# Kernel optimization log

Measured on AMD Instinct MI355X. Metric: run time of the kernel, lower is better.

The kernel has to match this reference:

```python
import jax, jax.numpy as jnp
import numpy as np

EMBED_DIM = 768
NUM_HEADS = 12
HEAD_DIM = EMBED_DIM // NUM_HEADS
KERNEL = 7


def _neighbor_index(size, kernel):
    # NATTEN border-clamped neighborhood: window start = clip(i - k//2, 0, size-k)
    start = np.clip(np.arange(size) - kernel // 2, 0, size - kernel)
    return jnp.asarray(start[:, None] + np.arange(kernel)[None, :])  # [size, kernel]


def setup_inputs() -> dict:
    key = jax.random.key(0)
    k1, k2, k3, k4, k5 = jax.random.split(key, 5)
    B, H, W, C = 8, 64, 64, EMBED_DIM
    x = jax.random.normal(k1, (B, H, W, C), dtype=jnp.float32)
    # torch.nn.Linear layout: weight [out, in]
    w_qkv = jax.random.normal(k2, (3 * C, C), dtype=jnp.float32) * (C ** -0.5)
    b_qkv = jax.random.normal(k3, (3 * C,), dtype=jnp.float32) * 0.02
    w_proj = jax.random.normal(k4, (C, C), dtype=jnp.float32) * (C ** -0.5)
    b_proj = jax.random.normal(k5, (C,), dtype=jnp.float32) * 0.02
    return {"x": x, "w_qkv": w_qkv, "b_qkv": b_qkv, "w_proj": w_proj, "b_proj": b_proj}


def reference(x, w_qkv, b_qkv, w_proj, b_proj):
    B, H, W, C = x.shape
    scale = HEAD_DIM ** -0.5
    qkv = (x @ w_qkv.T + b_qkv).reshape(B, H, W, 3, NUM_HEADS, HEAD_DIM)
    q = qkv[..., 0, :, :] * scale          # [B,H,W,nh,hd]
    k = qkv[..., 1, :, :]
    v = qkv[..., 2, :, :]

    idx_i = _neighbor_index(H, KERNEL)      # [H,K]
    idx_j = _neighbor_index(W, KERNEL)      # [W,K]

    # Logits over the K*K local neighborhood, one shifted gather per offset
    # (avoids materializing [B,H,W,K2,nh,hd]).
    logits = []
    for ki in range(KERNEL):
        k_row = jnp.take(k, idx_i[:, ki], axis=1)          # [B,H,W,nh,hd]
        for kj in range(KERNEL):
            k_nb = jnp.take(k_row, idx_j[:, kj], axis=2)   # [B,H,W,nh,hd]
            logits.append(jnp.einsum('bhwnd,bhwnd->bhwn', q, k_nb))
    logits = jnp.stack(logits, axis=-1)                     # [B,H,W,nh,K2]
    attn = jax.nn.softmax(logits, axis=-1)

    out = jnp.zeros((B, H, W, NUM_HEADS, HEAD_DIM), dtype=x.dtype)
    off = 0
    for ki in range(KERNEL):
        v_row = jnp.take(v, idx_i[:, ki], axis=1)
        for kj in range(KERNEL):
            v_nb = jnp.take(v_row, idx_j[:, kj], axis=2)
            out = out + attn[..., off][..., None] * v_nb
            off += 1

    out = out.reshape(B, H, W, C)
    return out @ w_proj.T + b_proj
```

## Files before the change

kernel.cpp:

```cpp
#include <hip/hip_runtime.h>
#include <cstddef>

#define EMBED   768
#define NHEADS  12
#define HDIM    64
#define KSZ     7
#define IMG_H   64
#define IMG_W   64
#define BATCH   8
#define NTOK    (BATCH*IMG_H*IMG_W)
#define QKV_N   (3*EMBED)

typedef __attribute__((ext_vector_type(8))) short  bf16x8;
typedef __attribute__((ext_vector_type(4))) float  f32x4;
typedef __attribute__((ext_vector_type(8))) unsigned short u16x8;
typedef __attribute__((ext_vector_type(4))) unsigned short u16x4;

__device__ __forceinline__ unsigned short f2bf(float f) {
    unsigned int u = __float_as_uint(f);
    u += 0x7FFFu + ((u >> 16) & 1u);
    return (unsigned short)(u >> 16);
}

__device__ __forceinline__ void gload_lds16(const void* g, void* l) {
    __builtin_amdgcn_global_load_lds(
        (const __attribute__((address_space(1))) unsigned int*)g,
        (__attribute__((address_space(3))) unsigned int*)l, 16, 0, 0);
}

__global__ __launch_bounds__(256)
void cvt_bf16_kernel(const float* __restrict__ in, unsigned short* __restrict__ out, int n4)
{
    int i = blockIdx.x * 256 + threadIdx.x;
    if (i < n4) {
        float4 f = *(const float4*)(in + (size_t)i * 4);
        u16x4 o;
        o[0] = f2bf(f.x); o[1] = f2bf(f.y); o[2] = f2bf(f.z); o[3] = f2bf(f.w);
        *(u16x4*)(out + (size_t)i * 4) = o;
    }
}

template<int BF16OUT>
__global__ __launch_bounds__(256)
void mfma_gemm(const unsigned short* __restrict__ A, const unsigned short* __restrict__ W,
               const float* __restrict__ bias, void* __restrict__ outp,
               int N, int K, int scaleN, float scale)
{
    __shared__ unsigned short As[128 * 32];
    __shared__ unsigned short Bs[128 * 32];
    const int t = threadIdx.x;
    const int l = t & 63, w = t >> 6;
    const int bm = blockIdx.x * 128, bn = blockIdx.y * 128;
    const int wr = (w >> 1) * 64, wc = (w & 1) * 64;

    f32x4 acc[4][4] = {};

    const int srow = t >> 2;
    const int scol = (t & 3) * 8;
    unsigned short* ldsA0 = As + w * 512;
    unsigned short* ldsA1 = As + 2048 + w * 512;
    unsigned short* ldsB0 = Bs + w * 512;
    unsigned short* ldsB1 = Bs + 2048 + w * 512;
    const unsigned short* gA0 = A + (size_t)(bm + srow) * K + scol;
    const unsigned short* gA1 = A + (size_t)(bm + 64 + srow) * K + scol;
    const unsigned short* gB0 = W + (size_t)(bn + srow) * K + scol;
    const unsigned short* gB1 = W + (size_t)(bn + 64 + srow) * K + scol;

    const unsigned short* ra = As + (size_t)(wr + (l & 15)) * 32 + (l >> 4) * 8;
    const unsigned short* rb = Bs + (size_t)(wc + (l & 15)) * 32 + (l >> 4) * 8;

    for (int k0 = 0; k0 < K; k0 += 32) {
        __syncthreads();
        gload_lds16(gA0 + k0, ldsA0);
        gload_lds16(gA1 + k0, ldsA1);
        gload_lds16(gB0 + k0, ldsB0);
        gload_lds16(gB1 + k0, ldsB1);
        __syncthreads();
        bf16x8 af[4], bfr[4];
        #pragma unroll
        for (int i = 0; i < 4; ++i) af[i]  = *(const bf16x8*)(ra + i * 16 * 32);
        #pragma unroll
        for (int j = 0; j < 4; ++j) bfr[j] = *(const bf16x8*)(rb + j * 16 * 32);
        #pragma unroll
        for (int i = 0; i < 4; ++i)
            #pragma unroll
            for (int j = 0; j < 4; ++j)
                acc[i][j] = __builtin_amdgcn_mfma_f32_16x16x32_bf16(af[i], bfr[j], acc[i][j], 0, 0, 0);
    }

    const int cr = (l >> 4) * 4;
    const int cc = l & 15;
    #pragma unroll
    for (int i = 0; i < 4; ++i) {
        #pragma unroll
        for (int j = 0; j < 4; ++j) {
            const int col = bn + wc + j * 16 + cc;
            const float bv = bias[col];
            const bool sc = col < scaleN;
            #pragma unroll
            for (int r = 0; r < 4; ++r) {
                const int row = bm + wr + i * 16 + cr + r;
                float v = acc[i][j][r] + bv;
                if (sc) v *= scale;
                if (BF16OUT) ((unsigned short*)outp)[(size_t)row * N + col] = f2bf(v);
                else         ((float*)outp)[(size_t)row * N + col] = v;
            }
        }
    }
}

__global__ __launch_bounds__(256)
void natten_kernel(const unsigned short* __restrict__ qkv, unsigned short* __restrict__ attn_bf)
{
    __shared__ unsigned short smem[4 * 5888];
    const int t = threadIdx.x;
    const int w = t >> 6, l = t & 63;
    const int c15 = l & 15, g = l >> 4;
    const int blk = blockIdx.x;
    const int tg = blk & 15;
    const int h = (blk >> 4) % NHEADS;
    const int b = blk / (16 * NHEADS);
    const int ti = (tg >> 2) * 16, tj = (tg & 3) * 16;
    const int pi0 = ti + w * 4;
    const int ws = min(max(pi0 - 3, 0), IMG_H - 10);
    const int cs = min(max(tj - 3, 0), IMG_W - 22);
    const int pixbase = b * 4096;

    unsigned short* Kl = smem + w * 5888;
    unsigned short* Vt = Kl + 2304;

    const int pj = tj + c15;
    const int sj = min(max(pj - 3, 0), IMG_W - KSZ);
    const unsigned int cm = 0x7Fu << (sj - cs);
    unsigned int rm[4];
    #pragma unroll
    for (int qt = 0; qt < 4; ++qt) {
        int si = min(max(pi0 + qt - 3, 0), IMG_H - KSZ);
        rm[qt] = 0x7Fu << (si - ws);
    }

    bf16x8 qf[4][2];
    #pragma unroll
    for (int qt = 0; qt < 4; ++qt)
        #pragma unroll
        for (int dh = 0; dh < 2; ++dh)
            qf[qt][dh] = *(const bf16x8*)(qkv +
                (size_t)(pixbase + (pi0 + qt) * 64 + tj + c15) * QKV_N + h * HDIM + dh * 32 + g * 8);

    const int sr = l & 31;
    const int h5 = l >> 5;
    const int sig = ((sr & 12) << 1) | ((sr & 16) >> 2) | (sr & 3);

    u16x8 kst[4], vst[4];

    {
        int ur = sr / 22, uc = sr - ur * 22;
        int prow = min(ws + ur, IMG_H - 1);
        const u16x8* gk = (const u16x8*)(qkv +
            (size_t)(pixbase + prow * 64 + cs + uc) * QKV_N + EMBED + h * HDIM + h5 * 32);
        #pragma unroll
        for (int i = 0; i < 4; ++i) { kst[i] = gk[i]; vst[i] = gk[i + 96]; }
    }
    #pragma unroll
    for (int i = 0; i < 4; ++i) *(u16x8*)(Kl + sr * 72 + h5 * 32 + i * 8) = kst[i];
    #pragma unroll
    for (int i = 0; i < 4; ++i)
        #pragma unroll
        for (int e = 0; e < 8; ++e)
            Vt[(h5 * 32 + i * 8 + e) * 56 + sig] = vst[i][e];

    f32x4 oacc[4][4] = {};
    float spart[4] = {0.f, 0.f, 0.f, 0.f};

    #pragma unroll 1
    for (int C = 0; C < 7; ++C) {
        if (C < 6) {
            int kk = (C + 1) * 32 + sr;
            int ur = kk / 22, uc = kk - ur * 22;
            int prow = min(ws + ur, IMG_H - 1);
            const u16x8* gk = (const u16x8*)(qkv +
                (size_t)(pixbase + prow * 64 + cs + uc) * QKV_N + EMBED + h * HDIM + h5 * 32);
            #pragma unroll
            for (int i = 0; i < 4; ++i) { kst[i] = gk[i]; vst[i] = gk[i + 96]; }
        }

        bf16x8 ka[2][2], vb[4];
        #pragma unroll
        for (int kt = 0; kt < 2; ++kt)
            #pragma unroll
            for (int dh = 0; dh < 2; ++dh)
                ka[kt][dh] = *(const bf16x8*)(Kl + (kt * 16 + c15) * 72 + dh * 32 + g * 8);
        #pragma unroll
        for (int dt = 0; dt < 4; ++dt)
            vb[dt] = *(const bf16x8*)(Vt + (dt * 16 + c15) * 56 + g * 8);

        int kk0 = C * 32 + 4 * g;
        int a22 = kk0 / 22;
        int uc0 = kk0 - a22 * 22;
        int urx[2][4]; unsigned int cb[2][4];
        #pragma unroll
        for (int kt = 0; kt < 2; ++kt)
            #pragma unroll
            for (int r = 0; r < 4; ++r) {
                int x = uc0 + kt * 16 + r;
                int wrp = x >= 22;
                int uc = x - (wrp ? 22 : 0);
                urx[kt][r] = a22 + wrp;
                cb[kt][r] = (cm >> uc) & 1u;
            }

        #pragma unroll
        for (int qt = 0; qt < 4; ++qt) {
            f32x4 s0 = {}, s1 = {};
            s0 = __builtin_amdgcn_mfma_f32_16x16x32_bf16(ka[0][0], qf[qt][0], s0, 0, 0, 0);
            s0 = __builtin_amdgcn_mfma_f32_16x16x32_bf16(ka[0][1], qf[qt][1], s0, 0, 0, 0);
            s1 = __builtin_amdgcn_mfma_f32_16x16x32_bf16(ka[1][0], qf[qt][0], s1, 0, 0, 0);
            s1 = __builtin_amdgcn_mfma_f32_16x16x32_bf16(ka[1][1], qf[qt][1], s1, 0, 0, 0);
            float p[2][4];
            #pragma unroll
            for (int r = 0; r < 4; ++r) {
                float e0 = exp2f(s0[r]);
                float e1 = exp2f(s1[r]);
                p[0][r] = ((rm[qt] >> urx[0][r]) & cb[0][r]) ? e0 : 0.f;
                p[1][r] = ((rm[qt] >> urx[1][r]) & cb[1][r]) ? e1 : 0.f;
                spart[qt] += p[0][r] + p[1][r];
            }
            unsigned int pk[4];
            asm("v_cvt_pk_bf16_f32 %0, %1, %2" : "=v"(pk[0]) : "v"(p[0][0]), "v"(p[0][1]));
            asm("v_cvt_pk_bf16_f32 %0, %1, %2" : "=v"(pk[1]) : "v"(p[0][2]), "v"(p[0][3]));
            asm("v_cvt_pk_bf16_f32 %0, %1, %2" : "=v"(pk[2]) : "v"(p[1][0]), "v"(p[1][1]));
            asm("v_cvt_pk_bf16_f32 %0, %1, %2" : "=v"(pk[3]) : "v"(p[1][2]), "v"(p[1][3]));
            bf16x8 pa = *(bf16x8*)pk;
            #pragma unroll
            for (int dt = 0; dt < 4; ++dt)
                oacc[qt][dt] = __builtin_amdgcn_mfma_f32_16x16x32_bf16(pa, vb[dt], oacc[qt][dt], 0, 0, 0);
        }

        if (C < 6) {
            #pragma unroll
            for (int i = 0; i < 4; ++i) *(u16x8*)(Kl + sr * 72 + h5 * 32 + i * 8) = kst[i];
            #pragma unroll
            for (int i = 0; i < 4; ++i)
                #pragma unroll
                for (int e = 0; e < 8; ++e)
                    Vt[(h5 * 32 + i * 8 + e) * 56 + sig] = vst[i][e];
        }
    }

    #pragma unroll
    for (int qt = 0; qt < 4; ++qt) {
        float s = spart[qt];
        s += __shfl_xor(s, 16);
        s += __shfl_xor(s, 32);
        #pragma unroll
        for (int r = 0; r < 4; ++r) {
            float sb = __shfl(s, 4 * g + r);
            float inv = __builtin_amdgcn_rcpf(sb);
            size_t obase = (size_t)(pixbase + (pi0 + qt) * 64 + tj + 4 * g + r) * EMBED
                         + h * HDIM + c15;
            #pragma unroll
            for (int dt = 0; dt < 4; ++dt)
                attn_bf[obase + dt * 16] = f2bf(oacc[qt][dt][r] * inv);
        }
    }
}

extern "C" void kernel_launch(void* const* d_in, const int* in_sizes, int n_in,
                              void* d_out, int out_size, void* d_ws, size_t ws_size,
                              hipStream_t stream)
{
    const float* x      = (const float*)d_in[0];
    const float* w_qkv  = (const float*)d_in[1];
    const float* b_qkv  = (const float*)d_in[2];
    const float* w_proj = (const float*)d_in[3];
    const float* b_proj = (const float*)d_in[4];
    float* out = (float*)d_out;

    char* p = (char*)d_ws;
    unsigned short* qkv = (unsigned short*)p;     p += (size_t)NTOK * QKV_N * 2;
    unsigned short* xbf = (unsigned short*)p;
    unsigned short* attn_bf = xbf;                p += (size_t)NTOK * EMBED * 2;
    unsigned short* wq_bf = (unsigned short*)p;   p += (size_t)QKV_N * EMBED * 2;
    unsigned short* wp_bf = (unsigned short*)p;

    const float scale = 0.125f * 1.44269504088896f;

    {
        int n4 = NTOK * EMBED / 4;
        cvt_bf16_kernel<<<(n4 + 255) / 256, 256, 0, stream>>>(x, xbf, n4);
        n4 = QKV_N * EMBED / 4;
        cvt_bf16_kernel<<<(n4 + 255) / 256, 256, 0, stream>>>(w_qkv, wq_bf, n4);
        n4 = EMBED * EMBED / 4;
        cvt_bf16_kernel<<<(n4 + 255) / 256, 256, 0, stream>>>(w_proj, wp_bf, n4);
    }

    {
        dim3 g1(NTOK / 128, QKV_N / 128);
        mfma_gemm<1><<<g1, 256, 0, stream>>>(xbf, wq_bf, b_qkv, qkv, QKV_N, EMBED, EMBED, scale);
    }

    natten_kernel<<<BATCH * NHEADS * 16, 256, 0, stream>>>(qkv, attn_bf);

    {
        dim3 g2(NTOK / 128, EMBED / 128);
        mfma_gemm<0><<<g2, 256, 0, stream>>>(attn_bf, wp_bf, b_proj, out, EMBED, EMBED, 0, 1.0f);
    }
}
```

Before: 359.1 us.

## Double-buffer GEMM LDS tiles and use lane-contiguous fragment layout

The MFMA GEMM now keeps two LDS buffers and prefetches the next K-slice through direct global-to-LDS loads while computing on the current one, so only one barrier per iteration is needed. The LDS layout also changes so that each 16-row fragment is stored lane-contiguously, letting each lane read its bf16x8 operand at l*8 and avoiding strided bank conflicts. In exchange, LDS use doubles, which may lower occupancy. Correctness depends on the async load into the other buffer being ordered against the trailing barrier.

```diff
diff --git a/kernel.cpp b/kernel.cpp
--- a/kernel.cpp
+++ b/kernel.cpp
@@ -46,46 +46,56 @@
                const float* __restrict__ bias, void* __restrict__ outp,
                int N, int K, int scaleN, float scale)
 {
-    __shared__ unsigned short As[128 * 32];
-    __shared__ unsigned short Bs[128 * 32];
+    __shared__ unsigned short As[2 * 4096];
+    __shared__ unsigned short Bs[2 * 4096];
     const int t = threadIdx.x;
     const int l = t & 63, w = t >> 6;
     const int bm = blockIdx.x * 128, bn = blockIdx.y * 128;
     const int wr = (w >> 1) * 64, wc = (w & 1) * 64;
 
+    const int r16 = l & 15, kg = l >> 4;
+    const unsigned short* gA0 = A + (size_t)(bm + w * 16 + r16) * K + kg * 8;
+    const unsigned short* gA1 = A + (size_t)(bm + (w + 4) * 16 + r16) * K + kg * 8;
+    const unsigned short* gB0 = W + (size_t)(bn + w * 16 + r16) * K + kg * 8;
+    const unsigned short* gB1 = W + (size_t)(bn + (w + 4) * 16 + r16) * K + kg * 8;
+    unsigned short* lA0 = As + w * 512;
+    unsigned short* lA1 = As + (w + 4) * 512;
+    unsigned short* lB0 = Bs + w * 512;
+    unsigned short* lB1 = Bs + (w + 4) * 512;
+
+    const unsigned short* ra = As + ((wr >> 4)) * 512 + l * 8;
+    const unsigned short* rb = Bs + ((wc >> 4)) * 512 + l * 8;
+
     f32x4 acc[4][4] = {};
-
-    const int srow = t >> 2;
-    const int scol = (t & 3) * 8;
-    unsigned short* ldsA0 = As + w * 512;
-    unsigned short* ldsA1 = As + 2048 + w * 512;
-    unsigned short* ldsB0 = Bs + w * 512;
-    unsigned short* ldsB1 = Bs + 2048 + w * 512;
-    const unsigned short* gA0 = A + (size_t)(bm + srow) * K + scol;
-    const unsigned short* gA1 = A + (size_t)(bm + 64 + srow) * K + scol;
-    const unsigned short* gB0 = W + (size_t)(bn + srow) * K + scol;
-    const unsigned short* gB1 = W + (size_t)(bn + 64 + srow) * K + scol;
-
-    const unsigned short* ra = As + (size_t)(wr + (l & 15)) * 32 + (l >> 4) * 8;
-    const unsigned short* rb = Bs + (size_t)(wc + (l & 15)) * 32 + (l >> 4) * 8;
-
-    for (int k0 = 0; k0 < K; k0 += 32) {
-        __syncthreads();
-        gload_lds16(gA0 + k0, ldsA0);
-        gload_lds16(gA1 + k0, ldsA1);
-        gload_lds16(gB0 + k0, ldsB0);
-        gload_lds16(gB1 + k0, ldsB1);
-        __syncthreads();
+    const int NT = K / 32;
+
+    gload_lds16(gA0, lA0);
+    gload_lds16(gA1, lA1);
+    gload_lds16(gB0, lB0);
+    gload_lds16(gB1, lB1);
+    __syncthreads();
+
+    for (int ts = 0; ts < NT; ++ts) {
+        const int cur = (ts & 1) * 4096;
+        if (ts + 1 < NT) {
+            const int nk = (ts + 1) * 32;
+            const int nb = ((ts + 1) & 1) * 4096;
+            gload_lds16(gA0 + nk, lA0 + nb);
+            gload_lds16(gA1 + nk, lA1 + nb);
+            gload_lds16(gB0 + nk, lB0 + nb);
+            gload_lds16(gB1 + nk, lB1 + nb);
+        }
         bf16x8 af[4], bfr[4];
         #pragma unroll
-        for (int i = 0; i < 4; ++i) af[i]  = *(const bf16x8*)(ra + i * 16 * 32);
-        #pragma unroll
-        for (int j = 0; j < 4; ++j) bfr[j] = *(const bf16x8*)(rb + j * 16 * 32);
+        for (int i = 0; i < 4; ++i) af[i]  = *(const bf16x8*)(ra + cur + i * 512);
+        #pragma unroll
+        for (int j = 0; j < 4; ++j) bfr[j] = *(const bf16x8*)(rb + cur + j * 512);
         #pragma unroll
         for (int i = 0; i < 4; ++i)
             #pragma unroll
             for (int j = 0; j < 4; ++j)
                 acc[i][j] = __builtin_amdgcn_mfma_f32_16x16x32_bf16(af[i], bfr[j], acc[i][j], 0, 0, 0);
+        __syncthreads();
     }
 
     const int cr = (l >> 4) * 4;
```

New measurement: 427.4 us. 1.19x slower.

## Replace GEMM with 256x256-tile triple-buffered pipelined MFMA kernel

Applied to the files above, without the earlier changes.

Replaces the 128x128 single-buffered GEMM with a 256x256 tile, 512-thread kernel. It uses a three-stage LDS ring with direct global-to-LDS prefetch two k-steps ahead, XOR swizzling against bank conflicts, split MFMA phases with s_setprio, and a swizzled block order for L2 locality. The aim is to hide global load latency behind MFMA work and raise arithmetic intensity for both projection GEMMs. In exchange it uses more registers and 96KB of LDS, and the synchronization relies on manual vmcnt waits.

```diff
diff --git a/kernel.cpp b/kernel.cpp
--- a/kernel.cpp
+++ b/kernel.cpp
@@ -41,66 +41,99 @@
 }
 
 template<int BF16OUT>
-__global__ __launch_bounds__(256)
-void mfma_gemm(const unsigned short* __restrict__ A, const unsigned short* __restrict__ W,
-               const float* __restrict__ bias, void* __restrict__ outp,
-               int N, int K, int scaleN, float scale)
+__global__ __launch_bounds__(512)
+void gemm256(const unsigned short* __restrict__ A, const unsigned short* __restrict__ W,
+             const float* __restrict__ bias, void* __restrict__ outp,
+             int M, int N, int K, int scaleN, float scale)
 {
-    __shared__ unsigned short As[128 * 32];
-    __shared__ unsigned short Bs[128 * 32];
-    const int t = threadIdx.x;
-    const int l = t & 63, w = t >> 6;
-    const int bm = blockIdx.x * 128, bn = blockIdx.y * 128;
-    const int wr = (w >> 1) * 64, wc = (w & 1) * 64;
-
-    f32x4 acc[4][4] = {};
-
-    const int srow = t >> 2;
-    const int scol = (t & 3) * 8;
-    unsigned short* ldsA0 = As + w * 512;
-    unsigned short* ldsA1 = As + 2048 + w * 512;
-    unsigned short* ldsB0 = Bs + w * 512;
-    unsigned short* ldsB1 = Bs + 2048 + w * 512;
-    const unsigned short* gA0 = A + (size_t)(bm + srow) * K + scol;
-    const unsigned short* gA1 = A + (size_t)(bm + 64 + srow) * K + scol;
-    const unsigned short* gB0 = W + (size_t)(bn + srow) * K + scol;
-    const unsigned short* gB1 = W + (size_t)(bn + 64 + srow) * K + scol;
-
-    const unsigned short* ra = As + (size_t)(wr + (l & 15)) * 32 + (l >> 4) * 8;
-    const unsigned short* rb = Bs + (size_t)(wc + (l & 15)) * 32 + (l >> 4) * 8;
-
-    for (int k0 = 0; k0 < K; k0 += 32) {
-        __syncthreads();
-        gload_lds16(gA0 + k0, ldsA0);
-        gload_lds16(gA1 + k0, ldsA1);
-        gload_lds16(gB0 + k0, ldsB0);
-        gload_lds16(gB1 + k0, ldsB1);
-        __syncthreads();
-        bf16x8 af[4], bfr[4];
-        #pragma unroll
-        for (int i = 0; i < 4; ++i) af[i]  = *(const bf16x8*)(ra + i * 16 * 32);
-        #pragma unroll
-        for (int j = 0; j < 4; ++j) bfr[j] = *(const bf16x8*)(rb + j * 16 * 32);
-        #pragma unroll
-        for (int i = 0; i < 4; ++i)
-            #pragma unroll
-            for (int j = 0; j < 4; ++j)
-                acc[i][j] = __builtin_amdgcn_mfma_f32_16x16x32_bf16(af[i], bfr[j], acc[i][j], 0, 0, 0);
+    __shared__ unsigned short lds[3 * 16384];
+    const int t_ = threadIdx.x;
+    const int l = t_ & 63, w = t_ >> 6;
+    const int wr2 = w >> 2, wc4 = w & 3;
+
+    const int nbx = M >> 8;
+    const int lin = blockIdx.x;
+    const int cpx = gridDim.x >> 3;
+    const int swz = (lin & 7) * cpx + (lin >> 3);
+    const int bm = (swz % nbx) << 8;
+    const int bn = (swz / nbx) << 8;
+
+    const int kperm = ((l & 3) ^ ((l >> 3) & 3)) * 8;
+    const unsigned short* gA = A + (size_t)(bm + w * 16 + (l >> 2)) * K + kperm;
+    const unsigned short* gB = W + (size_t)(bn + w * 16 + (l >> 2)) * K + kperm;
+    const size_t step8 = (size_t)128 * K;
+
+    unsigned short* lA = lds + w * 512;
+    unsigned short* lB = lds + 8192 + w * 512;
+
+    const int foff = (l & 15) * 32 + (((l >> 4) ^ ((l >> 1) & 3)) * 8);
+    const unsigned short* raw = lds + (wr2 * 8) * 512 + foff;
+    const unsigned short* rbw = lds + 8192 + (wc4 * 4) * 512 + foff;
+
+    f32x4 acc[8][4] = {};
+    const int NT = K / 32;
+
+    gload_lds16(gA, lA);              gload_lds16(gA + step8, lA + 4096);
+    gload_lds16(gB, lB);              gload_lds16(gB + step8, lB + 4096);
+    gload_lds16(gA + 32, lA + 16384); gload_lds16(gA + step8 + 32, lA + 16384 + 4096);
+    gload_lds16(gB + 32, lB + 16384); gload_lds16(gB + step8 + 32, lB + 16384 + 4096);
+    asm volatile("s_waitcnt vmcnt(4)" ::: "memory");
+    __builtin_amdgcn_s_barrier();
+
+    for (int t = 0; t < NT; ++t) {
+        const int q  = (t % 3) * 16384;
+        const int qn = ((t + 2) % 3) * 16384;
+        const bool pf = (t + 2 < NT);
+        const int ko = t * 32 + 64;
+
+        if (pf) { gload_lds16(gA + ko, lA + qn); gload_lds16(gA + step8 + ko, lA + qn + 4096); }
+        bf16x8 af0[4], bf[4];
+        #pragma unroll
+        for (int m = 0; m < 4; ++m) af0[m] = *(const bf16x8*)(raw + q + m * 512);
+        #pragma unroll
+        for (int n = 0; n < 4; ++n) bf[n]  = *(const bf16x8*)(rbw + q + n * 512);
+        __builtin_amdgcn_s_barrier();
+        __builtin_amdgcn_s_setprio(1);
+        #pragma unroll
+        for (int m = 0; m < 4; ++m)
+            #pragma unroll
+            for (int n = 0; n < 4; ++n)
+                acc[m][n] = __builtin_amdgcn_mfma_f32_16x16x32_bf16(af0[m], bf[n], acc[m][n], 0, 0, 0);
+        __builtin_amdgcn_s_setprio(0);
+        __builtin_amdgcn_s_barrier();
+
+        if (pf) { gload_lds16(gB + ko, lB + qn); gload_lds16(gB + step8 + ko, lB + qn + 4096); }
+        bf16x8 af1[4];
+        #pragma unroll
+        for (int m = 0; m < 4; ++m) af1[m] = *(const bf16x8*)(raw + q + (4 + m) * 512);
+        __builtin_amdgcn_s_barrier();
+        __builtin_amdgcn_s_setprio(1);
+        #pragma unroll
+        for (int m = 0; m < 4; ++m)
+            #pragma unroll
+            for (int n = 0; n < 4; ++n)
+                acc[4 + m][n] = __builtin_amdgcn_mfma_f32_16x16x32_bf16(af1[m], bf[n], acc[4 + m][n], 0, 0, 0);
+        __builtin_amdgcn_s_setprio(0);
+        if (t < NT - 1) {
+            if (pf) asm volatile("s_waitcnt vmcnt(4)" ::: "memory");
+            else    asm volatile("s_waitcnt vmcnt(0)" ::: "memory");
+            __builtin_amdgcn_s_barrier();
+        }
     }
 
     const int cr = (l >> 4) * 4;
     const int cc = l & 15;
     #pragma unroll
-    for (int i = 0; i < 4; ++i) {
-        #pragma unroll
-        for (int j = 0; j < 4; ++j) {
-            const int col = bn + wc + j * 16 + cc;
+    for (int m = 0; m < 8; ++m) {
+        #pragma unroll
+        for (int n = 0; n < 4; ++n) {
+            const int col = bn + wc4 * 64 + n * 16 + cc;
             const float bv = bias[col];
             const bool sc = col < scaleN;
             #pragma unroll
             for (int r = 0; r < 4; ++r) {
-                const int row = bm + wr + i * 16 + cr + r;
-                float v = acc[i][j][r] + bv;
+                const int row = bm + wr2 * 128 + m * 16 + cr + r;
+                float v = acc[m][n][r] + bv;
                 if (sc) v *= scale;
                 if (BF16OUT) ((unsigned short*)outp)[(size_t)row * N + col] = f2bf(v);
                 else         ((float*)outp)[(size_t)row * N + col] = v;
@@ -295,14 +328,14 @@
     }
 
     {
-        dim3 g1(NTOK / 128, QKV_N / 128);
-        mfma_gemm<1><<<g1, 256, 0, stream>>>(xbf, wq_bf, b_qkv, qkv, QKV_N, EMBED, EMBED, scale);
+        gemm256<1><<<(NTOK / 256) * (QKV_N / 256), 512, 0, stream>>>(
+            xbf, wq_bf, b_qkv, qkv, NTOK, QKV_N, EMBED, EMBED, scale);
     }
 
     natten_kernel<<<BATCH * NHEADS * 16, 256, 0, stream>>>(qkv, attn_bf);
 
     {
-        dim3 g2(NTOK / 128, EMBED / 128);
-        mfma_gemm<0><<<g2, 256, 0, stream>>>(attn_bf, wp_bf, b_proj, out, EMBED, EMBED, 0, 1.0f);
-    }
-}
+        gemm256<0><<<(NTOK / 256) * (EMBED / 256), 512, 0, stream>>>(
+            attn_bf, wp_bf, b_proj, out, NTOK, EMBED, EMBED, 0, 1.0f);
+    }
+}
```

New measurement: 337.5 us. 1.06x faster.
